# Optimization experiments

Hardware: AMD Instinct MI355X
Metric: run time of the kernel (lower is better)

Reference implementation:

```python
import jax, jax.numpy as jnp
import numpy as np
import math

B, N, D_POINTS, D_MODEL, K = 4, 4096, 512, 256, 16


def _gather(points, idx):
    # points: [B, N, C], idx: [B, S, K] -> [B, S, K, C]
    return jax.vmap(lambda p, i: p[i])(points, idx)


def setup_inputs() -> dict:
    key = jax.random.key(0)
    ks = jax.random.split(key, 20)
    def lin(k_, fan_in, fan_out):
        lim = 1.0 / math.sqrt(fan_in)
        return jax.random.uniform(k_, (fan_in, fan_out), jnp.float32, -lim, lim)
    inp = {
        "xyz": jax.random.normal(ks[0], (B, N, 3), jnp.float32),
        "features": jax.random.normal(ks[1], (B, N, D_POINTS), jnp.float32),
        # fc1: d_points -> d_model
        "W1": lin(ks[2], D_POINTS, D_MODEL), "b1": jnp.zeros((D_MODEL,), jnp.float32),
        # fc2: d_model -> d_points
        "W2": lin(ks[3], D_MODEL, D_POINTS), "b2": jnp.zeros((D_POINTS,), jnp.float32),
        # fc_delta: 3 -> d_model -> d_model
        "Wd1": lin(ks[4], 3, D_MODEL), "bd1": jnp.zeros((D_MODEL,), jnp.float32),
        "Wd2": lin(ks[5], D_MODEL, D_MODEL), "bd2": jnp.zeros((D_MODEL,), jnp.float32),
        # fc_gamma: d_model -> d_model -> d_model
        "Wg1": lin(ks[6], D_MODEL, D_MODEL), "bg1": jnp.zeros((D_MODEL,), jnp.float32),
        "Wg2": lin(ks[7], D_MODEL, D_MODEL), "bg2": jnp.zeros((D_MODEL,), jnp.float32),
        # q/k/v projections (no bias)
        "Wq": lin(ks[8], D_MODEL, D_MODEL),
        "Wk": lin(ks[9], D_MODEL, D_MODEL),
        "Wv": lin(ks[10], D_MODEL, D_MODEL),
        "k": K,
    }
    return inp


def reference(xyz, features, W1, b1, W2, b2, Wd1, bd1, Wd2, bd2,
              Wg1, bg1, Wg2, bg2, Wq, Wk, Wv, k):
    # pairwise squared distances [B, N, N]
    sq = jnp.sum(xyz * xyz, axis=-1)
    dists = sq[:, :, None] + sq[:, None, :] - 2.0 * jnp.einsum('bnc,bmc->bnm', xyz, xyz)
    _, knn_idx = jax.lax.top_k(-dists, k)              # [B, N, k] nearest (incl. self)
    knn_xyz = _gather(xyz, knn_idx)                    # [B, N, k, 3]

    pre = features
    x = features @ W1 + b1                             # [B, N, d_model]
    q = x @ Wq                                         # [B, N, d_model]
    kk = _gather(x @ Wk, knn_idx)                      # [B, N, k, d_model]
    v = _gather(x @ Wv, knn_idx)                       # [B, N, k, d_model]

    rel = xyz[:, :, None, :] - knn_xyz                 # [B, N, k, 3]
    pos_enc = jax.nn.relu(rel @ Wd1 + bd1) @ Wd2 + bd2 # [B, N, k, d_model]

    h = q[:, :, None, :] - kk + pos_enc
    attn = jax.nn.relu(h @ Wg1 + bg1) @ Wg2 + bg2      # [B, N, k, d_model]
    attn = jax.nn.softmax(attn / math.sqrt(D_MODEL), axis=-2)  # over k neighbors

    res = jnp.einsum('bnkf,bnkf->bnf', attn, v + pos_enc)
    res = res @ W2 + b2 + pre                          # [B, N, d_points]
    return res, attn
```

## Files before the change

kernel.cpp:

```cpp
#include <hip/hip_runtime.h>
#include <hip/hip_bf16.h>
#include <stdint.h>

typedef __hip_bfloat16 bf16;
typedef float f32x4 __attribute__((ext_vector_type(4)));
typedef __bf16 bf16x8 __attribute__((ext_vector_type(8)));

__device__ __forceinline__ float b2f(bf16 v) { return __bfloat162float(v); }
__device__ __forceinline__ bf16 f2b(float v) { return __float2bfloat16(v); }
__device__ __forceinline__ unsigned short f2bu(float f) {
  unsigned u = __float_as_uint(f);
  unsigned r = u + 0x7fffu + ((u >> 16) & 1u);
  return (unsigned short)(r >> 16);
}


#define CE64(a, b)                                            \
  do {                                                        \
    bool c_ = (b) < (a);                                      \
    unsigned long long lo_ = c_ ? (b) : (a);                  \
    unsigned long long hi_ = c_ ? (a) : (b);                  \
    (a) = lo_; (b) = hi_;                                     \
  } while (0)

__global__ __launch_bounds__(256) void pack_pts(const float* __restrict__ xyz,
                                                float4* __restrict__ pts) {
  int i = blockIdx.x * 256 + threadIdx.x;
  float x = xyz[i * 3 + 0];
  float y = xyz[i * 3 + 1];
  float z = xyz[i * 3 + 2];
  float sq = __fadd_rn(__fadd_rn(__fmul_rn(x, x), __fmul_rn(y, y)), __fmul_rn(z, z));
  pts[i] = make_float4(x, y, z, sq);
}

__global__ __launch_bounds__(256) void knn_partial(const float4* __restrict__ pts,
                                                   unsigned long long* __restrict__ keys) {
  __shared__ __align__(16) float4 cs[1024];
  __shared__ __align__(16) float4 qs[64];

  int tid = threadIdx.x;
  int g = blockIdx.x >> 2;
  int r = blockIdx.x & 3;
  int batch = g >> 6;
  const float4* pp = pts + batch * 4096;
  int cb = r * 1024;

#pragma unroll
  for (int i = 0; i < 4; ++i) cs[i * 256 + tid] = pp[cb + i * 256 + tid];
  if (tid < 64) qs[tid] = pp[(g & 63) * 64 + tid];
  __syncthreads();

  int wave = tid >> 6, lq = tid & 63;
  float4 Q = qs[lq];
  int mbase = cb + wave * 256;

  unsigned long long k0 = ~0ull, k1 = ~0ull, k2 = ~0ull, k3 = ~0ull;
  unsigned long long k4 = ~0ull, k5 = ~0ull, k6 = ~0ull, k7 = ~0ull;
  unsigned long long k8 = ~0ull, k9 = ~0ull, k10 = ~0ull, k11 = ~0ull;
  unsigned long long k12 = ~0ull, k13 = ~0ull, k14 = ~0ull, k15 = ~0ull;

  for (int t = 0; t < 256; ++t) {
    float4 P = cs[wave * 256 + t];
    float dot = __fadd_rn(__fadd_rn(__fmul_rn(Q.x, P.x), __fmul_rn(Q.y, P.y)),
                          __fmul_rn(Q.z, P.z));
    float d = __fsub_rn(__fadd_rn(Q.w, P.w), __fmul_rn(2.0f, dot));
    unsigned u = __float_as_uint(d);
    u ^= (unsigned)((int)u >> 31) | 0x80000000u;
    unsigned long long nk = ((unsigned long long)u << 32) | (unsigned)(mbase + t);
    if (nk < k15) {
      k15 = nk;
      CE64(k14, k15); CE64(k13, k14); CE64(k12, k13); CE64(k11, k12);
      CE64(k10, k11); CE64(k9, k10);  CE64(k8, k9);   CE64(k7, k8);
      CE64(k6, k7);   CE64(k5, k6);   CE64(k4, k5);   CE64(k3, k4);
      CE64(k2, k3);   CE64(k1, k2);   CE64(k0, k1);
    }
  }

  int rw = r * 4 + wave;
  int q = g * 64 + lq;
  unsigned long long* o = keys + (size_t)(rw * 16) * 16384 + q;
  o[0] = k0;           o[16384] = k1;       o[2 * 16384] = k2;   o[3 * 16384] = k3;
  o[4 * 16384] = k4;   o[5 * 16384] = k5;   o[6 * 16384] = k6;   o[7 * 16384] = k7;
  o[8 * 16384] = k8;   o[9 * 16384] = k9;   o[10 * 16384] = k10; o[11 * 16384] = k11;
  o[12 * 16384] = k12; o[13 * 16384] = k13; o[14 * 16384] = k14; o[15 * 16384] = k15;
}

__global__ __launch_bounds__(256) void knn_merge(const unsigned long long* __restrict__ keys,
                                                 int* __restrict__ gidx) {
  int q = blockIdx.x * 256 + threadIdx.x;
  const unsigned long long* kq = keys + q;

#define LOADL(rw)                                   \
  unsigned long long l0 = kq[((rw) * 16 + 0) * 16384],  l1 = kq[((rw) * 16 + 1) * 16384],  \
                     l2 = kq[((rw) * 16 + 2) * 16384],  l3 = kq[((rw) * 16 + 3) * 16384],  \
                     l4 = kq[((rw) * 16 + 4) * 16384],  l5 = kq[((rw) * 16 + 5) * 16384],  \
                     l6 = kq[((rw) * 16 + 6) * 16384],  l7 = kq[((rw) * 16 + 7) * 16384],  \
                     l8 = kq[((rw) * 16 + 8) * 16384],  l9 = kq[((rw) * 16 + 9) * 16384],  \
                     l10 = kq[((rw) * 16 + 10) * 16384], l11 = kq[((rw) * 16 + 11) * 16384], \
                     l12 = kq[((rw) * 16 + 12) * 16384], l13 = kq[((rw) * 16 + 13) * 16384], \
                     l14 = kq[((rw) * 16 + 14) * 16384], l15 = kq[((rw) * 16 + 15) * 16384]

  unsigned long long a0 = kq[0],           a1 = kq[16384],      a2 = kq[2 * 16384],
                     a3 = kq[3 * 16384],   a4 = kq[4 * 16384],  a5 = kq[5 * 16384],
                     a6 = kq[6 * 16384],   a7 = kq[7 * 16384],  a8 = kq[8 * 16384],
                     a9 = kq[9 * 16384],   a10 = kq[10 * 16384], a11 = kq[11 * 16384],
                     a12 = kq[12 * 16384], a13 = kq[13 * 16384], a14 = kq[14 * 16384],
                     a15 = kq[15 * 16384];

  for (int rw = 1; rw < 16; ++rw) {
    LOADL(rw);
    a0 = a0 < l15 ? a0 : l15;   a1 = a1 < l14 ? a1 : l14;
    a2 = a2 < l13 ? a2 : l13;   a3 = a3 < l12 ? a3 : l12;
    a4 = a4 < l11 ? a4 : l11;   a5 = a5 < l10 ? a5 : l10;
    a6 = a6 < l9 ? a6 : l9;     a7 = a7 < l8 ? a7 : l8;
    a8 = a8 < l7 ? a8 : l7;     a9 = a9 < l6 ? a9 : l6;
    a10 = a10 < l5 ? a10 : l5;  a11 = a11 < l4 ? a11 : l4;
    a12 = a12 < l3 ? a12 : l3;  a13 = a13 < l2 ? a13 : l2;
    a14 = a14 < l1 ? a14 : l1;  a15 = a15 < l0 ? a15 : l0;
    CE64(a0, a8);  CE64(a1, a9);  CE64(a2, a10); CE64(a3, a11);
    CE64(a4, a12); CE64(a5, a13); CE64(a6, a14); CE64(a7, a15);
    CE64(a0, a4);  CE64(a1, a5);  CE64(a2, a6);  CE64(a3, a7);
    CE64(a8, a12); CE64(a9, a13); CE64(a10, a14); CE64(a11, a15);
    CE64(a0, a2);  CE64(a1, a3);  CE64(a4, a6);  CE64(a5, a7);
    CE64(a8, a10); CE64(a9, a11); CE64(a12, a14); CE64(a13, a15);
    CE64(a0, a1);  CE64(a2, a3);  CE64(a4, a5);  CE64(a6, a7);
    CE64(a8, a9);  CE64(a10, a11); CE64(a12, a13); CE64(a14, a15);
  }
#undef LOADL

  int base = (q >> 12) << 12;
  int* o = gidx + (size_t)q * 16;
  o[0] = base + (int)(a0 & 0xffffffffu);   o[1] = base + (int)(a1 & 0xffffffffu);
  o[2] = base + (int)(a2 & 0xffffffffu);   o[3] = base + (int)(a3 & 0xffffffffu);
  o[4] = base + (int)(a4 & 0xffffffffu);   o[5] = base + (int)(a5 & 0xffffffffu);
  o[6] = base + (int)(a6 & 0xffffffffu);   o[7] = base + (int)(a7 & 0xffffffffu);
  o[8] = base + (int)(a8 & 0xffffffffu);   o[9] = base + (int)(a9 & 0xffffffffu);
  o[10] = base + (int)(a10 & 0xffffffffu); o[11] = base + (int)(a11 & 0xffffffffu);
  o[12] = base + (int)(a12 & 0xffffffffu); o[13] = base + (int)(a13 & 0xffffffffu);
  o[14] = base + (int)(a14 & 0xffffffffu); o[15] = base + (int)(a15 & 0xffffffffu);
}

__global__ __launch_bounds__(256) void transpose_k(const float* __restrict__ src,
                                                   bf16* __restrict__ dst,
                                                   int R, int C) {
  int i = blockIdx.x * 256 + threadIdx.x;
  if (i < R * C) {
    int r = i / C, c = i - r * C;
    dst[c * R + r] = f2b(src[i]);
  }
}

__global__ __launch_bounds__(256) void hidden_kernel(const float* __restrict__ xyz,
                                                     const int* __restrict__ gidx,
                                                     const float* __restrict__ Wd1,
                                                     const float* __restrict__ bd1,
                                                     bf16* __restrict__ hidden) {
  __shared__ float rel[16][3];
  int q = blockIdx.x;
  int tid = threadIdx.x;
  if (tid < 16) {
    int g = gidx[q * 16 + tid];
    rel[tid][0] = xyz[(size_t)q * 3 + 0] - xyz[(size_t)g * 3 + 0];
    rel[tid][1] = xyz[(size_t)q * 3 + 1] - xyz[(size_t)g * 3 + 1];
    rel[tid][2] = xyz[(size_t)q * 3 + 2] - xyz[(size_t)g * 3 + 2];
  }
  __syncthreads();
  float w0 = Wd1[tid], w1 = Wd1[256 + tid], w2 = Wd1[512 + tid];
  float bb = bd1[tid];
#pragma unroll
  for (int j = 0; j < 16; ++j) {
    float v = rel[j][0] * w0 + rel[j][1] * w1 + rel[j][2] * w2 + bb;
    v = fmaxf(v, 0.0f);
    hidden[((size_t)q * 16 + j) * 256 + tid] = f2b(v);
  }
}

template <int EPI, typename AT, typename CT>
__global__ __launch_bounds__(256) void gemm_bt(
    const AT* __restrict__ A, const bf16* __restrict__ BT,
    const float* __restrict__ bias, CT* __restrict__ C,
    int M, int N, int K,
    const bf16* __restrict__ e0p, const bf16* __restrict__ e1p,
    const bf16* __restrict__ e2p, const int* __restrict__ gidx,
    bf16* __restrict__ o1, const float* __restrict__ resid) {
  __shared__ __align__(16) unsigned short As[128 * 72];
  __shared__ __align__(16) unsigned short Bs[128 * 72];

  int ntn = N >> 7;
  int bx = blockIdx.x % ntn, by = blockIdx.x / ntn;
  int m0 = by * 128, n0 = bx * 128;
  int tid = threadIdx.x;
  int wave = tid >> 6, lane = tid & 63;
  int wr = wave >> 1, wc = wave & 1;
  int lm = lane & 15, lqd = lane >> 4;

  f32x4 acc[4][4] = {};

  for (int k0 = 0; k0 < K; k0 += 64) {
#pragma unroll
    for (int i = 0; i < 4; ++i) {
      int flat = i * 256 + tid;
      int row = flat >> 3;
      int u = flat & 7;
      if constexpr (sizeof(AT) == 4) {
        const float* ap = (const float*)A + (size_t)(m0 + row) * K + k0 + u * 8;
        float4 a0 = *reinterpret_cast<const float4*>(ap);
        float4 a1 = *reinterpret_cast<const float4*>(ap + 4);
        unsigned short* dst = &As[row * 72 + u * 8];
        dst[0] = f2bu(a0.x); dst[1] = f2bu(a0.y); dst[2] = f2bu(a0.z); dst[3] = f2bu(a0.w);
        dst[4] = f2bu(a1.x); dst[5] = f2bu(a1.y); dst[6] = f2bu(a1.z); dst[7] = f2bu(a1.w);
      } else {
        int4 av = *reinterpret_cast<const int4*>((const bf16*)A + (size_t)(m0 + row) * K + k0 + u * 8);
        *reinterpret_cast<int4*>(&As[row * 72 + u * 8]) = av;
      }
      int4 bv = *reinterpret_cast<const int4*>(BT + (size_t)(n0 + row) * K + k0 + u * 8);
      *reinterpret_cast<int4*>(&Bs[row * 72 + u * 8]) = bv;
    }
    __syncthreads();
#pragma unroll
    for (int ks = 0; ks < 2; ++ks) {
      bf16x8 af[4], bfr[4];
#pragma unroll
      for (int mi = 0; mi < 4; ++mi)
        af[mi] = *reinterpret_cast<const bf16x8*>(
            &As[(wr * 64 + mi * 16 + lm) * 72 + ks * 32 + lqd * 8]);
#pragma unroll
      for (int ni = 0; ni < 4; ++ni)
        bfr[ni] = *reinterpret_cast<const bf16x8*>(
            &Bs[(wc * 64 + ni * 16 + lm) * 72 + ks * 32 + lqd * 8]);
#pragma unroll
      for (int mi = 0; mi < 4; ++mi)
#pragma unroll
        for (int ni = 0; ni < 4; ++ni)
          acc[mi][ni] = __builtin_amdgcn_mfma_f32_16x16x32_bf16(af[mi], bfr[ni],
                                                                acc[mi][ni], 0, 0, 0);
    }
    __syncthreads();
  }

#pragma unroll
  for (int mi = 0; mi < 4; ++mi) {
    int mbase = m0 + wr * 64 + mi * 16;
#pragma unroll
    for (int ni = 0; ni < 4; ++ni) {
      int n = n0 + wc * 64 + ni * 16 + lm;
      float bv = bias ? bias[n] : 0.0f;
      if constexpr (EPI == 3) {
        float l0 = acc[mi][ni][0] + bv, l1 = acc[mi][ni][1] + bv;
        float l2 = acc[mi][ni][2] + bv, l3 = acc[mi][ni][3] + bv;
        float mx = fmaxf(fmaxf(l0, l1), fmaxf(l2, l3));
        mx = fmaxf(mx, __shfl_xor(mx, 16, 64));
        mx = fmaxf(mx, __shfl_xor(mx, 32, 64));
        float ev[4];
        ev[0] = __expf((l0 - mx) * 0.0625f);
        ev[1] = __expf((l1 - mx) * 0.0625f);
        ev[2] = __expf((l2 - mx) * 0.0625f);
        ev[3] = __expf((l3 - mx) * 0.0625f);
        float s = ev[0] + ev[1] + ev[2] + ev[3];
        s += __shfl_xor(s, 16, 64);
        s += __shfl_xor(s, 32, 64);
        float inv = 1.0f / s;
        float rp = 0.0f;
#pragma unroll
        for (int r = 0; r < 4; ++r) {
          size_t m = (size_t)(mbase + lqd * 4 + r);
          float a = ev[r] * inv;
          C[m * 256 + n] = a;
          rp += a * b2f(e2p[m * 256 + n]);
        }
        rp += __shfl_xor(rp, 16, 64);
        rp += __shfl_xor(rp, 32, 64);
        if (lqd == 0) o1[(size_t)(mbase >> 4) * 256 + n] = f2b(rp);
      } else {
#pragma unroll
        for (int r = 0; r < 4; ++r) {
          size_t m = (size_t)(mbase + lqd * 4 + r);
          float v = acc[mi][ni][r] + bv;
          if constexpr (EPI == 1) v = fmaxf(v, 0.0f);
          if constexpr (EPI == 2) {
            int g = gidx[m];
            float qv = b2f(e0p[(m >> 4) * (size_t)256 + n]);
            float kv = b2f(e1p[(size_t)g * 256 + n]);
            float vv = b2f(e2p[(size_t)g * 256 + n]);
            C[m * (size_t)N + n] = f2b(qv - kv + v);
            o1[m * (size_t)N + n] = f2b(vv + v);
          } else if constexpr (EPI == 4) {
            v += resid[m * (size_t)N + n];
            C[m * (size_t)N + n] = v;
          } else {
            C[m * (size_t)N + n] = f2b(v);
          }
        }
      }
    }
  }
}

extern "C" void kernel_launch(void* const* d_in, const int* in_sizes, int n_in,
                              void* d_out, int out_size, void* d_ws, size_t ws_size,
                              hipStream_t stream) {
  const float* xyz = (const float*)d_in[0];
  const float* feat = (const float*)d_in[1];
  const float* W1 = (const float*)d_in[2];
  const float* b1 = (const float*)d_in[3];
  const float* W2 = (const float*)d_in[4];
  const float* b2 = (const float*)d_in[5];
  const float* Wd1 = (const float*)d_in[6];
  const float* bd1 = (const float*)d_in[7];
  const float* Wd2 = (const float*)d_in[8];
  const float* bd2 = (const float*)d_in[9];
  const float* Wg1 = (const float*)d_in[10];
  const float* bg1 = (const float*)d_in[11];
  const float* Wg2 = (const float*)d_in[12];
  const float* bg2 = (const float*)d_in[13];
  const float* Wq = (const float*)d_in[14];
  const float* Wk = (const float*)d_in[15];
  const float* Wv = (const float*)d_in[16];

  constexpr size_t XBUF = 0;
  constexpr size_t QBUF = 8388608;
  constexpr size_t KBUF = 16777216;
  constexpr size_t VBUF = 25165824;
  constexpr size_t RESPRE = 33554432;
  constexpr size_t GIDX = 41943040;
  constexpr size_t W1T = 42991616;
  constexpr size_t W2T = 43253760;
  constexpr size_t WQT = 43515904;
  constexpr size_t WKT = 43646976;
  constexpr size_t WVT = 43778048;
  constexpr size_t WD2T = 43909120;
  constexpr size_t WG1T = 44040192;
  constexpr size_t WG2T = 44171264;
  constexpr size_t HIDDEN = 44302336;
  constexpr size_t HBUF = 178520064;
  constexpr size_t VPBUF = 312737792;
  constexpr size_t WS_NEEDED = 446955520;
  if (ws_size < WS_NEEDED) return;

  char* ws = (char*)d_ws;
  bf16* xbuf = (bf16*)(ws + XBUF);
  bf16* qbuf = (bf16*)(ws + QBUF);
  bf16* kbuf = (bf16*)(ws + KBUF);
  bf16* vbuf = (bf16*)(ws + VBUF);
  bf16* respre = (bf16*)(ws + RESPRE);
  int* gidx = (int*)(ws + GIDX);
  bf16* w1t = (bf16*)(ws + W1T);
  bf16* w2t = (bf16*)(ws + W2T);
  bf16* wqt = (bf16*)(ws + WQT);
  bf16* wkt = (bf16*)(ws + WKT);
  bf16* wvt = (bf16*)(ws + WVT);
  bf16* wd2t = (bf16*)(ws + WD2T);
  bf16* wg1t = (bf16*)(ws + WG1T);
  bf16* wg2t = (bf16*)(ws + WG2T);
  bf16* hidden = (bf16*)(ws + HIDDEN);
  bf16* hbuf = (bf16*)(ws + HBUF);
  bf16* vpbuf = (bf16*)(ws + VPBUF);

  unsigned long long* knnkeys = (unsigned long long*)(ws + HBUF);
  float4* pts4 = (float4*)(ws + HBUF + 33554432);

  float* res_out = (float*)d_out;
  float* attn_out = res_out + (size_t)16384 * 512;

  transpose_k<<<512, 256, 0, stream>>>(W1, w1t, 512, 256);
  transpose_k<<<512, 256, 0, stream>>>(W2, w2t, 256, 512);
  transpose_k<<<256, 256, 0, stream>>>(Wq, wqt, 256, 256);
  transpose_k<<<256, 256, 0, stream>>>(Wk, wkt, 256, 256);
  transpose_k<<<256, 256, 0, stream>>>(Wv, wvt, 256, 256);
  transpose_k<<<256, 256, 0, stream>>>(Wd2, wd2t, 256, 256);
  transpose_k<<<256, 256, 0, stream>>>(Wg1, wg1t, 256, 256);
  transpose_k<<<256, 256, 0, stream>>>(Wg2, wg2t, 256, 256);

  pack_pts<<<64, 256, 0, stream>>>(xyz, pts4);
  knn_partial<<<1024, 256, 0, stream>>>(pts4, knnkeys);
  knn_merge<<<64, 256, 0, stream>>>(knnkeys, gidx);

  gemm_bt<0, float, bf16><<<128 * 2, 256, 0, stream>>>(
      feat, w1t, b1, xbuf, 16384, 256, 512,
      nullptr, nullptr, nullptr, nullptr, nullptr, nullptr);
  gemm_bt<0, bf16, bf16><<<128 * 2, 256, 0, stream>>>(
      xbuf, wqt, nullptr, qbuf, 16384, 256, 256,
      nullptr, nullptr, nullptr, nullptr, nullptr, nullptr);
  gemm_bt<0, bf16, bf16><<<128 * 2, 256, 0, stream>>>(
      xbuf, wkt, nullptr, kbuf, 16384, 256, 256,
      nullptr, nullptr, nullptr, nullptr, nullptr, nullptr);
  gemm_bt<0, bf16, bf16><<<128 * 2, 256, 0, stream>>>(
      xbuf, wvt, nullptr, vbuf, 16384, 256, 256,
      nullptr, nullptr, nullptr, nullptr, nullptr, nullptr);

  hidden_kernel<<<16384, 256, 0, stream>>>(xyz, gidx, Wd1, bd1, hidden);

  gemm_bt<2, bf16, bf16><<<2048 * 2, 256, 0, stream>>>(
      hidden, wd2t, bd2, hbuf, 262144, 256, 256,
      qbuf, kbuf, vbuf, gidx, vpbuf, nullptr);
  gemm_bt<1, bf16, bf16><<<2048 * 2, 256, 0, stream>>>(
      hbuf, wg1t, bg1, hidden, 262144, 256, 256,
      nullptr, nullptr, nullptr, nullptr, nullptr, nullptr);
  gemm_bt<3, bf16, float><<<2048 * 2, 256, 0, stream>>>(
      hidden, wg2t, bg2, attn_out, 262144, 256, 256,
      nullptr, nullptr, vpbuf, nullptr, respre, nullptr);
  gemm_bt<4, bf16, float><<<128 * 4, 256, 0, stream>>>(
      respre, w2t, b2, res_out, 16384, 512, 256,
      nullptr, nullptr, nullptr, nullptr, nullptr, feat);
}
```

Baseline: 1.164 ms.

## Batch KNN candidates with bitonic sort-merge and split candidates across more blocks

knn_partial now splits each query's candidates into 8 chunks of 512 instead of 4 of 1024, doubling the grid and the number of partial lists. Each wave sorts candidates in groups of 8 with a bitonic network and merges them into its top-16 through a branch-free bitonic merge, replacing the per-candidate insertion that diverges across the wave. knn_merge now merges 32 partial lists, and the key buffer doubles, so the packed-points offset moves. The trade is more merge work and more key traffic through memory in exchange for fixed, divergence-free sorting and more parallelism.

```diff
diff --git a/kernel.cpp b/kernel.cpp
--- a/kernel.cpp
+++ b/kernel.cpp
@@ -21,6 +21,13 @@
     unsigned long long lo_ = c_ ? (b) : (a);                  \
     unsigned long long hi_ = c_ ? (a) : (b);                  \
     (a) = lo_; (b) = hi_;                                     \
+  } while (0)
+
+#define CEA(x, y) CE64(x, y)
+#define CED(x, y) CE64(y, x)
+#define MIN64(x, y)                                           \
+  do {                                                        \
+    (x) = (y) < (x) ? (y) : (x);                              \
   } while (0)
 
 __global__ __launch_bounds__(256) void pack_pts(const float* __restrict__ xyz,
@@ -35,54 +42,68 @@
 
 __global__ __launch_bounds__(256) void knn_partial(const float4* __restrict__ pts,
                                                    unsigned long long* __restrict__ keys) {
-  __shared__ __align__(16) float4 cs[1024];
+  __shared__ __align__(16) float4 cs[512];
   __shared__ __align__(16) float4 qs[64];
 
   int tid = threadIdx.x;
-  int g = blockIdx.x >> 2;
-  int r = blockIdx.x & 3;
+  int g = blockIdx.x >> 3;
+  int r = blockIdx.x & 7;
   int batch = g >> 6;
   const float4* pp = pts + batch * 4096;
-  int cb = r * 1024;
-
-#pragma unroll
-  for (int i = 0; i < 4; ++i) cs[i * 256 + tid] = pp[cb + i * 256 + tid];
+  int cb = r * 512;
+
+  cs[tid] = pp[cb + tid];
+  cs[256 + tid] = pp[cb + 256 + tid];
   if (tid < 64) qs[tid] = pp[(g & 63) * 64 + tid];
   __syncthreads();
 
   int wave = tid >> 6, lq = tid & 63;
   float4 Q = qs[lq];
-  int mbase = cb + wave * 256;
-
-  unsigned long long k0 = ~0ull, k1 = ~0ull, k2 = ~0ull, k3 = ~0ull;
-  unsigned long long k4 = ~0ull, k5 = ~0ull, k6 = ~0ull, k7 = ~0ull;
-  unsigned long long k8 = ~0ull, k9 = ~0ull, k10 = ~0ull, k11 = ~0ull;
-  unsigned long long k12 = ~0ull, k13 = ~0ull, k14 = ~0ull, k15 = ~0ull;
-
-  for (int t = 0; t < 256; ++t) {
-    float4 P = cs[wave * 256 + t];
-    float dot = __fadd_rn(__fadd_rn(__fmul_rn(Q.x, P.x), __fmul_rn(Q.y, P.y)),
-                          __fmul_rn(Q.z, P.z));
-    float d = __fsub_rn(__fadd_rn(Q.w, P.w), __fmul_rn(2.0f, dot));
-    unsigned u = __float_as_uint(d);
-    u ^= (unsigned)((int)u >> 31) | 0x80000000u;
-    unsigned long long nk = ((unsigned long long)u << 32) | (unsigned)(mbase + t);
-    if (nk < k15) {
-      k15 = nk;
-      CE64(k14, k15); CE64(k13, k14); CE64(k12, k13); CE64(k11, k12);
-      CE64(k10, k11); CE64(k9, k10);  CE64(k8, k9);   CE64(k7, k8);
-      CE64(k6, k7);   CE64(k5, k6);   CE64(k4, k5);   CE64(k3, k4);
-      CE64(k2, k3);   CE64(k1, k2);   CE64(k0, k1);
+  int mbase = cb + wave * 128;
+
+  unsigned long long a[16];
+#pragma unroll
+  for (int i = 0; i < 16; ++i) a[i] = ~0ull;
+
+#pragma unroll 2
+  for (int tb = 0; tb < 16; ++tb) {
+    unsigned long long c[8];
+#pragma unroll
+    for (int j = 0; j < 8; ++j) {
+      float4 P = cs[wave * 128 + tb * 8 + j];
+      float dot = __fadd_rn(__fadd_rn(__fmul_rn(Q.x, P.x), __fmul_rn(Q.y, P.y)),
+                            __fmul_rn(Q.z, P.z));
+      float d = __fsub_rn(__fadd_rn(Q.w, P.w), __fmul_rn(2.0f, dot));
+      unsigned u = __float_as_uint(d);
+      u ^= (unsigned)((int)u >> 31) | 0x80000000u;
+      c[j] = ((unsigned long long)u << 32) | (unsigned)(mbase + tb * 8 + j);
     }
+
+    CEA(c[0], c[1]); CED(c[2], c[3]); CEA(c[4], c[5]); CED(c[6], c[7]);
+    CEA(c[0], c[2]); CEA(c[1], c[3]); CED(c[4], c[6]); CED(c[5], c[7]);
+    CEA(c[0], c[1]); CEA(c[2], c[3]); CED(c[4], c[5]); CED(c[6], c[7]);
+    CEA(c[0], c[4]); CEA(c[1], c[5]); CEA(c[2], c[6]); CEA(c[3], c[7]);
+    CEA(c[0], c[2]); CEA(c[1], c[3]); CEA(c[4], c[6]); CEA(c[5], c[7]);
+    CEA(c[0], c[1]); CEA(c[2], c[3]); CEA(c[4], c[5]); CEA(c[6], c[7]);
+
+    MIN64(a[8],  c[7]); MIN64(a[9],  c[6]); MIN64(a[10], c[5]); MIN64(a[11], c[4]);
+    MIN64(a[12], c[3]); MIN64(a[13], c[2]); MIN64(a[14], c[1]); MIN64(a[15], c[0]);
+
+    CEA(a[0], a[8]);  CEA(a[1], a[9]);  CEA(a[2], a[10]); CEA(a[3], a[11]);
+    CEA(a[4], a[12]); CEA(a[5], a[13]); CEA(a[6], a[14]); CEA(a[7], a[15]);
+    CEA(a[0], a[4]);  CEA(a[1], a[5]);  CEA(a[2], a[6]);  CEA(a[3], a[7]);
+    CEA(a[8], a[12]); CEA(a[9], a[13]); CEA(a[10], a[14]); CEA(a[11], a[15]);
+    CEA(a[0], a[2]);  CEA(a[1], a[3]);  CEA(a[4], a[6]);  CEA(a[5], a[7]);
+    CEA(a[8], a[10]); CEA(a[9], a[11]); CEA(a[12], a[14]); CEA(a[13], a[15]);
+    CEA(a[0], a[1]);  CEA(a[2], a[3]);  CEA(a[4], a[5]);  CEA(a[6], a[7]);
+    CEA(a[8], a[9]);  CEA(a[10], a[11]); CEA(a[12], a[13]); CEA(a[14], a[15]);
   }
 
   int rw = r * 4 + wave;
   int q = g * 64 + lq;
   unsigned long long* o = keys + (size_t)(rw * 16) * 16384 + q;
-  o[0] = k0;           o[16384] = k1;       o[2 * 16384] = k2;   o[3 * 16384] = k3;
-  o[4 * 16384] = k4;   o[5 * 16384] = k5;   o[6 * 16384] = k6;   o[7 * 16384] = k7;
-  o[8 * 16384] = k8;   o[9 * 16384] = k9;   o[10 * 16384] = k10; o[11 * 16384] = k11;
-  o[12 * 16384] = k12; o[13 * 16384] = k13; o[14 * 16384] = k14; o[15 * 16384] = k15;
+#pragma unroll
+  for (int j = 0; j < 16; ++j) o[(size_t)j * 16384] = a[j];
 }
 
 __global__ __launch_bounds__(256) void knn_merge(const unsigned long long* __restrict__ keys,
@@ -107,7 +128,7 @@
                      a12 = kq[12 * 16384], a13 = kq[13 * 16384], a14 = kq[14 * 16384],
                      a15 = kq[15 * 16384];
 
-  for (int rw = 1; rw < 16; ++rw) {
+  for (int rw = 1; rw < 32; ++rw) {
     LOADL(rw);
     a0 = a0 < l15 ? a0 : l15;   a1 = a1 < l14 ? a1 : l14;
     a2 = a2 < l13 ? a2 : l13;   a3 = a3 < l12 ? a3 : l12;
@@ -357,7 +378,7 @@
   bf16* vpbuf = (bf16*)(ws + VPBUF);
 
   unsigned long long* knnkeys = (unsigned long long*)(ws + HBUF);
-  float4* pts4 = (float4*)(ws + HBUF + 33554432);
+  float4* pts4 = (float4*)(ws + HBUF + 67108864);
 
   float* res_out = (float*)d_out;
   float* attn_out = res_out + (size_t)16384 * 512;
@@ -372,7 +393,7 @@
   transpose_k<<<256, 256, 0, stream>>>(Wg2, wg2t, 256, 256);
 
   pack_pts<<<64, 256, 0, stream>>>(xyz, pts4);
-  knn_partial<<<1024, 256, 0, stream>>>(pts4, knnkeys);
+  knn_partial<<<2048, 256, 0, stream>>>(pts4, knnkeys);
   knn_merge<<<64, 256, 0, stream>>>(knnkeys, gidx);
 
   gemm_bt<0, float, bf16><<<128 * 2, 256, 0, stream>>>(
```

Result: faster. 1.036 ms (-11.0%).
